# Kernel tuning notes

Hardware: AMD Instinct MI355X
Metric: run time of the kernel (lower is better)

## Reference

```python
import jax, jax.numpy as jnp
import numpy as np

B, S, E, H, SN, LMAX = 128, 512, 768, 16, 100, 5
DH = E // H  # 48

def setup_inputs() -> dict:
    key = jax.random.key(0)
    ks = jax.random.split(key, 10)
    idx = jax.random.randint(ks[0], (B, LMAX), 0, S)
    lengths = jax.random.randint(ks[1], (B,), 1, LMAX + 1)
    valid = jnp.arange(LMAX)[None, :] < lengths[:, None]
    locations = jnp.where(valid, idx, -1)
    return {
        "last_hidden_state": jax.random.normal(ks[2], (B, S, E), jnp.float32),
        "sense_emb": jax.random.normal(ks[3], (B, SN, E), jnp.float32),
        "locations": locations,
        "in_proj_weight": jax.random.normal(ks[4], (3 * E, E), jnp.float32) * 0.02,
        "in_proj_bias": jax.random.normal(ks[5], (3 * E,), jnp.float32) * 0.02,
        "out_proj_weight": jax.random.normal(ks[6], (E, E), jnp.float32) * 0.02,
        "out_proj_bias": jax.random.normal(ks[7], (E,), jnp.float32) * 0.02,
        "linear_weight": jax.random.normal(ks[8], (SN, E), jnp.float32) * 0.02,
        "linear_bias": jax.random.normal(ks[9], (SN,), jnp.float32) * 0.02,
    }

def reference(last_hidden_state, sense_emb, locations, in_proj_weight, in_proj_bias,
              out_proj_weight, out_proj_bias, linear_weight, linear_bias):
    # Ragged gather + mean over the valid (non -1) token locations per row.
    mask = (locations != -1)                                   # [B, LMAX]
    safe = jnp.where(mask, locations, 0)                       # [B, LMAX]
    gathered = jnp.take_along_axis(last_hidden_state, safe[..., None], axis=1)  # [B,LMAX,E]
    cnt = mask.sum(axis=1, keepdims=True).astype(last_hidden_state.dtype)
    pun = (gathered * mask[..., None]).sum(axis=1) / cnt       # [B, E]

    # qkv: prepend pun-word embedding to the sense embeddings -> [B, SN+1, E]
    qkv = jnp.concatenate([pun[:, None, :], sense_emb], axis=1)

    # nn.MultiheadAttention with batch_first=False: axis0 = seq (L=B), axis1 = batch (N=SN+1).
    proj = qkv @ in_proj_weight.T + in_proj_bias               # [L, N, 3E]
    q, k, v = jnp.split(proj, 3, axis=-1)
    L, N = qkv.shape[0], qkv.shape[1]
    q = q.reshape(L, N, H, DH) * (DH ** -0.5)
    k = k.reshape(L, N, H, DH)
    v = v.reshape(L, N, H, DH)
    scores = jnp.einsum('lnhd,mnhd->nhlm', q, k)               # [N,H,L,L]
    attn = jax.nn.softmax(scores, axis=-1)
    ctx = jnp.einsum('nhlm,mnhd->lnhd', attn, v).reshape(L, N, E)
    attn_out = ctx @ out_proj_weight.T + out_proj_bias         # [L, N, E]

    res = attn_out[:, 0, :]                                    # [B, E] (batch slot 0)
    res = res @ linear_weight.T + linear_bias                  # [B, SN]
    return res
```

## Files before the change

### kernel.cpp

```cpp
#include <hip/hip_runtime.h>

#define SEQ 512
#define EMB 768
#define K3E 2304
#define DHD 48

__global__ __launch_bounds__(256) void k0_pun(
    const float* __restrict__ lhs, const int* __restrict__ loc,
    float* __restrict__ pun)
{
  int id = blockIdx.x * 256 + threadIdx.x;
  int row = id / 192;
  int ch  = id - row * 192;
  int cnt = 0;
  float4 s = make_float4(0.f, 0.f, 0.f, 0.f);
#pragma unroll
  for (int j = 0; j < 5; j++) {
    int v = loc[row * 5 + j];
    if (v >= 0) {
      float4 wv = *(const float4*)&lhs[((size_t)row * SEQ + v) * EMB + ch * 4];
      s.x += wv.x; s.y += wv.y; s.z += wv.z; s.w += wv.w;
      cnt++;
    }
  }
  float inv = 1.0f / (float)cnt;
  *(float4*)&pun[(size_t)row * EMB + ch * 4] =
      make_float4(s.x * inv, s.y * inv, s.z * inv, s.w * inv);
}

__global__ __launch_bounds__(512, 4) void k1_gemm_wcomb(
    const float* __restrict__ pun, const float* __restrict__ Bw,
    const float* __restrict__ bias, float* __restrict__ C,
    const float* __restrict__ wlin, const float* __restrict__ wout,
    float* __restrict__ wcomb)
{
  __shared__ float lds[14336];
  const int t = threadIdx.x;
  const int w = t >> 6, l = t & 63;
  const int tx = l & 7, ty = l >> 3;
  const int gm = l & 15, gq = l >> 4;
  const int kbase = w * 96;
  const int AW = w * 1792, BW = AW + 640;

  float4 aF, bF0, bF1;
  float acc[2][4] = {};

#define STAGE_A(b) {                                                         \
    int Ab = AW + (b) * 320;                                                 \
    lds[Ab + (gq*4+0)*20 + gm] = aF.x;                                       \
    lds[Ab + (gq*4+1)*20 + gm] = aF.y;                                       \
    lds[Ab + (gq*4+2)*20 + gm] = aF.z;                                       \
    lds[Ab + (gq*4+3)*20 + gm] = aF.w; }

#define INNER(b) {                                                           \
    int Ab = AW + (b) * 320, Bb = BW + (b) * 576;                            \
    _Pragma("unroll")                                                        \
    for (int kk = 0; kk < 16; kk++) {                                        \
      float2 a  = *(float2*)&lds[Ab + kk * 20 + ty * 2];                     \
      float4 bb = *(float4*)&lds[Bb + kk * 36 + tx * 4];                     \
      acc[0][0] += a.x*bb.x; acc[0][1] += a.x*bb.y;                          \
      acc[0][2] += a.x*bb.z; acc[0][3] += a.x*bb.w;                          \
      acc[1][0] += a.y*bb.x; acc[1][1] += a.y*bb.y;                          \
      acc[1][2] += a.y*bb.z; acc[1][3] += a.y*bb.w;                          \
    } }

  if (blockIdx.x < 576) {
    const int c  = blockIdx.x;
    const int bm = (c / 72) * 16, bn = (c % 72) * 32;
    const int bl = l & 31, bh = l >> 5;
    const float* arow = pun + (size_t)(bm + gm) * EMB;
    const float* brow = Bw + (size_t)(bn + bl) * EMB;

#define G_LOAD(s) {                                                          \
    int k0 = kbase + (s) * 16;                                               \
    aF  = *(const float4*)&arow[k0 + gq * 4];                                \
    bF0 = *(const float4*)&brow[k0 + bh * 8 + 0];                            \
    bF1 = *(const float4*)&brow[k0 + bh * 8 + 4]; }

#define G_WRITE(b) {                                                         \
    STAGE_A(b)                                                               \
    int Bb = BW + (b) * 576;                                                 \
    lds[Bb + (bh*8+0)*36 + bl] = bF0.x; lds[Bb + (bh*8+1)*36 + bl] = bF0.y;  \
    lds[Bb + (bh*8+2)*36 + bl] = bF0.z; lds[Bb + (bh*8+3)*36 + bl] = bF0.w;  \
    lds[Bb + (bh*8+4)*36 + bl] = bF1.x; lds[Bb + (bh*8+5)*36 + bl] = bF1.y;  \
    lds[Bb + (bh*8+6)*36 + bl] = bF1.z; lds[Bb + (bh*8+7)*36 + bl] = bF1.w; }

    G_LOAD(0); G_WRITE(0);
    for (int s = 0; s < 6; s++) {
      int b = s & 1;
      if (s < 5) G_LOAD(s + 1);
      INNER(b);
      if (s < 5) G_WRITE(b ^ 1);
    }
#undef G_LOAD
#undef G_WRITE

#pragma unroll
    for (int i = 0; i < 2; i++)
      *(float4*)&lds[AW + (ty*2 + i) * 32 + tx * 4] =
          make_float4(acc[i][0], acc[i][1], acc[i][2], acc[i][3]);
    __syncthreads();
    int m = t >> 5, n = t & 31;
    float v = lds[0*1792 + t] + lds[1*1792 + t] + lds[2*1792 + t] + lds[3*1792 + t]
            + lds[4*1792 + t] + lds[5*1792 + t] + lds[6*1792 + t] + lds[7*1792 + t]
            + bias[bn + n];
    C[(size_t)(bm + m) * K3E + bn + n] = v;
  } else {
    const int cc = blockIdx.x - 576;
    const int bm = (cc / 24) * 16, bn = (cc % 24) * 32;
    const int wi = l >> 2;
    const int j4 = (l & 3) * 8;
    int arow_i = bm + gm; if (arow_i > 99) arow_i = 99;
    const float* arow = wlin + (size_t)arow_i * EMB;

#define W_LOAD(s) {                                                          \
    int k0 = kbase + (s) * 16;                                               \
    aF  = *(const float4*)&arow[k0 + gq * 4];                                \
    const float* wr = wout + (size_t)(k0 + wi) * EMB + bn + j4;              \
    bF0 = *(const float4*)&wr[0];                                            \
    bF1 = *(const float4*)&wr[4]; }

#define W_WRITE(b) {                                                         \
    STAGE_A(b)                                                               \
    int Bb = BW + (b) * 576;                                                 \
    *(float4*)&lds[Bb + wi*36 + j4]     = bF0;                               \
    *(float4*)&lds[Bb + wi*36 + j4 + 4] = bF1; }

    W_LOAD(0); W_WRITE(0);
    for (int s = 0; s < 6; s++) {
      int b = s & 1;
      if (s < 5) W_LOAD(s + 1);
      INNER(b);
      if (s < 5) W_WRITE(b ^ 1);
    }
#undef W_LOAD
#undef W_WRITE

#pragma unroll
    for (int i = 0; i < 2; i++)
      *(float4*)&lds[AW + (ty*2 + i) * 32 + tx * 4] =
          make_float4(acc[i][0], acc[i][1], acc[i][2], acc[i][3]);
    __syncthreads();
    int m = t >> 5, n = t & 31;
    if (bm + m < 100) {
      float v = lds[0*1792 + t] + lds[1*1792 + t] + lds[2*1792 + t] + lds[3*1792 + t]
              + lds[4*1792 + t] + lds[5*1792 + t] + lds[6*1792 + t] + lds[7*1792 + t];
      wcomb[(size_t)(bm + m) * EMB + bn + n] = v;
    }
  }
#undef STAGE_A
#undef INNER
}

__global__ __launch_bounds__(256) void k2_attn(
    const float* __restrict__ proj, float* __restrict__ ctx)
{
  __shared__ float ks[128][52];
  __shared__ float vs[128][52];
  int h  = blockIdx.x >> 3;
  int l0 = (blockIdx.x & 7) * 16;
  int t  = threadIdx.x;

  for (int i = t; i < 128 * 12; i += 256) {
    int m  = i / 12;
    int dd = (i - m * 12) * 4;
    float4 kv = *(const float4*)&proj[(size_t)m * K3E + EMB     + h * DHD + dd];
    float4 vv = *(const float4*)&proj[(size_t)m * K3E + 2 * EMB + h * DHD + dd];
    *(float4*)&ks[m][dd] = kv;
    *(float4*)&vs[m][dd] = vv;
  }

  int l  = t >> 4;
  int g  = t & 15;
  int lg = l0 + l;
  const float scale = 0.14433756729740643f;
  float q[48];
#pragma unroll
  for (int jj = 0; jj < 12; jj++) {
    float4 qv = *(const float4*)&proj[(size_t)lg * K3E + h * DHD + jj * 4];
    q[jj*4+0] = qv.x * scale; q[jj*4+1] = qv.y * scale;
    q[jj*4+2] = qv.z * scale; q[jj*4+3] = qv.w * scale;
  }
  __syncthreads();

  float sv[8];
  float smax = -1e30f;
#pragma unroll
  for (int jm = 0; jm < 8; jm++) {
    int m = g + jm * 16;
    float s = 0.0f;
#pragma unroll
    for (int dq = 0; dq < 12; dq++) {
      float4 kv = *(const float4*)&ks[m][dq * 4];
      s += q[dq*4+0]*kv.x + q[dq*4+1]*kv.y + q[dq*4+2]*kv.z + q[dq*4+3]*kv.w;
    }
    sv[jm] = s;
    smax = fmaxf(smax, s);
  }
#pragma unroll
  for (int off = 1; off < 16; off <<= 1) smax = fmaxf(smax, __shfl_xor(smax, off));
  float ssum = 0.0f;
#pragma unroll
  for (int jm = 0; jm < 8; jm++) { float e = __expf(sv[jm] - smax); sv[jm] = e; ssum += e; }
#pragma unroll
  for (int off = 1; off < 16; off <<= 1) ssum += __shfl_xor(ssum, off);
  float inv = 1.0f / ssum;
#pragma unroll
  for (int jm = 0; jm < 8; jm++) sv[jm] *= inv;

  float acc[48] = {};
#pragma unroll
  for (int jm = 0; jm < 8; jm++) {
    int m = g + jm * 16;
    float p = sv[jm];
#pragma unroll
    for (int dq = 0; dq < 12; dq++) {
      float4 vv = *(const float4*)&vs[m][dq * 4];
      acc[dq*4+0] += p*vv.x; acc[dq*4+1] += p*vv.y;
      acc[dq*4+2] += p*vv.z; acc[dq*4+3] += p*vv.w;
    }
  }

  {
    float buf[24];
    if (g & 8) {
#pragma unroll
      for (int d = 0; d < 24; d++) buf[d] = acc[d];
    } else {
#pragma unroll
      for (int d = 0; d < 24; d++) buf[d] = acc[d + 24];
    }
#pragma unroll
    for (int d = 0; d < 24; d++) buf[d] = __shfl_xor(buf[d], 8);
    if (g & 8) {
#pragma unroll
      for (int d = 0; d < 24; d++) acc[d] = acc[d + 24] + buf[d];
    } else {
#pragma unroll
      for (int d = 0; d < 24; d++) acc[d] = acc[d] + buf[d];
    }
  }
  {
    float buf[12];
    if (g & 4) {
#pragma unroll
      for (int d = 0; d < 12; d++) buf[d] = acc[d];
    } else {
#pragma unroll
      for (int d = 0; d < 12; d++) buf[d] = acc[d + 12];
    }
#pragma unroll
    for (int d = 0; d < 12; d++) buf[d] = __shfl_xor(buf[d], 4);
    if (g & 4) {
#pragma unroll
      for (int d = 0; d < 12; d++) acc[d] = acc[d + 12] + buf[d];
    } else {
#pragma unroll
      for (int d = 0; d < 12; d++) acc[d] = acc[d] + buf[d];
    }
  }
  {
    float buf[6];
    if (g & 2) {
#pragma unroll
      for (int d = 0; d < 6; d++) buf[d] = acc[d];
    } else {
#pragma unroll
      for (int d = 0; d < 6; d++) buf[d] = acc[d + 6];
    }
#pragma unroll
    for (int d = 0; d < 6; d++) buf[d] = __shfl_xor(buf[d], 2);
    if (g & 2) {
#pragma unroll
      for (int d = 0; d < 6; d++) acc[d] = acc[d + 6] + buf[d];
    } else {
#pragma unroll
      for (int d = 0; d < 6; d++) acc[d] = acc[d] + buf[d];
    }
  }
  {
    float buf[3];
    if (g & 1) {
#pragma unroll
      for (int d = 0; d < 3; d++) buf[d] = acc[d];
    } else {
#pragma unroll
      for (int d = 0; d < 3; d++) buf[d] = acc[d + 3];
    }
#pragma unroll
    for (int d = 0; d < 3; d++) buf[d] = __shfl_xor(buf[d], 1);
    if (g & 1) {
#pragma unroll
      for (int d = 0; d < 3; d++) acc[d] = acc[d + 3] + buf[d];
    } else {
#pragma unroll
      for (int d = 0; d < 3; d++) acc[d] = acc[d] + buf[d];
    }
  }
#pragma unroll
  for (int j = 0; j < 3; j++) {
    ctx[(size_t)lg * EMB + h * DHD + g * 3 + j] = acc[j];
  }
}

__global__ __launch_bounds__(512, 4) void k3_final(
    const float* __restrict__ A, const float* __restrict__ Bw,
    const float* __restrict__ wlin, const float* __restrict__ bout,
    const float* __restrict__ blin, float* __restrict__ C)
{
  __shared__ float lds[14368];
  const int t = threadIdx.x;
  const int w = t >> 6, l = t & 63;
  const int bm = blockIdx.y * 16, bn = blockIdx.x * 32;
  const int tx = l & 7, ty = l >> 3;
  const int gm = l & 15, gq = l >> 4;
  const int bl = l & 31, bh = l >> 5;
  const int kbase = w * 96;
  const int AW = w * 1792, BW = AW + 640;

  if (t < 256) {
    int col = bn + (t >> 3);
    int ks  = (t & 7) * 96;
    float p = 0.f;
    if (col < 100) {
      const float* wr = wlin + (size_t)col * EMB + ks;
#pragma unroll
      for (int j = 0; j < 24; j++) {
        float4 wv = *(const float4*)&wr[j * 4];
        float4 bv = *(const float4*)&bout[ks + j * 4];
        p += wv.x*bv.x + wv.y*bv.y + wv.z*bv.z + wv.w*bv.w;
      }
    }
    p += __shfl_xor(p, 1); p += __shfl_xor(p, 2); p += __shfl_xor(p, 4);
    if ((t & 7) == 0) lds[14336 + (t >> 3)] = p + (col < 100 ? blin[col] : 0.f);
  }

  const float* arow = A + (size_t)(bm + gm) * EMB;
  int brow_i = bn + bl; if (brow_i > 99) brow_i = 99;
  const float* brow = Bw + (size_t)brow_i * EMB;

  float4 aF, bF0, bF1;

#define F_LOAD(s) {                                                          \
    int k0 = kbase + (s) * 16;                                               \
    aF  = *(const float4*)&arow[k0 + gq * 4];                                \
    bF0 = *(const float4*)&brow[k0 + bh * 8 + 0];                            \
    bF1 = *(const float4*)&brow[k0 + bh * 8 + 4]; }

#define F_WRITE(b) {                                                         \
    int Ab = AW + (b) * 320;                                                 \
    lds[Ab + (gq*4+0)*20 + gm] = aF.x;                                       \
    lds[Ab + (gq*4+1)*20 + gm] = aF.y;                                       \
    lds[Ab + (gq*4+2)*20 + gm] = aF.z;                                       \
    lds[Ab + (gq*4+3)*20 + gm] = aF.w;                                       \
    int Bb = BW + (b) * 576;                                                 \
    lds[Bb + (bh*8+0)*36 + bl] = bF0.x; lds[Bb + (bh*8+1)*36 + bl] = bF0.y;  \
    lds[Bb + (bh*8+2)*36 + bl] = bF0.z; lds[Bb + (bh*8+3)*36 + bl] = bF0.w;  \
    lds[Bb + (bh*8+4)*36 + bl] = bF1.x; lds[Bb + (bh*8+5)*36 + bl] = bF1.y;  \
    lds[Bb + (bh*8+6)*36 + bl] = bF1.z; lds[Bb + (bh*8+7)*36 + bl] = bF1.w; }

  float acc[2][4] = {};
  F_LOAD(0); F_WRITE(0);
  for (int s = 0; s < 6; s++) {
    int b = s & 1;
    if (s < 5) F_LOAD(s + 1);
    int Ab = AW + b * 320, Bb = BW + b * 576;
#pragma unroll
    for (int kk = 0; kk < 16; kk++) {
      float2 a  = *(float2*)&lds[Ab + kk * 20 + ty * 2];
      float4 bb = *(float4*)&lds[Bb + kk * 36 + tx * 4];
      acc[0][0] += a.x*bb.x; acc[0][1] += a.x*bb.y; acc[0][2] += a.x*bb.z; acc[0][3] += a.x*bb.w;
      acc[1][0] += a.y*bb.x; acc[1][1] += a.y*bb.y; acc[1][2] += a.y*bb.z; acc[1][3] += a.y*bb.w;
    }
    if (s < 5) F_WRITE(b ^ 1);
  }
#undef F_LOAD
#undef F_WRITE

#pragma unroll
  for (int i = 0; i < 2; i++)
    *(float4*)&lds[AW + (ty*2 + i) * 32 + tx * 4] =
        make_float4(acc[i][0], acc[i][1], acc[i][2], acc[i][3]);
  __syncthreads();
  int m = t >> 5, n = t & 31;
  int col = bn + n;
  if (col < 100) {
    float v = lds[0*1792 + t] + lds[1*1792 + t] + lds[2*1792 + t] + lds[3*1792 + t]
            + lds[4*1792 + t] + lds[5*1792 + t] + lds[6*1792 + t] + lds[7*1792 + t]
            + lds[14336 + n];
    C[(size_t)(bm + m) * 100 + col] = v;
  }
}

extern "C" void kernel_launch(void* const* d_in, const int* in_sizes, int n_in,
                              void* d_out, int out_size, void* d_ws, size_t ws_size,
                              hipStream_t stream) {
  const float* lhs   = (const float*)d_in[0];
  const int*   loc   = (const int*)  d_in[2];
  const float* w_in  = (const float*)d_in[3];
  const float* b_in  = (const float*)d_in[4];
  const float* w_out = (const float*)d_in[5];
  const float* b_out = (const float*)d_in[6];
  const float* w_lin = (const float*)d_in[7];
  const float* b_lin = (const float*)d_in[8];
  float* out = (float*)d_out;

  char* ws = (char*)d_ws;
  float* pun   = (float*)(ws);
  float* proj  = (float*)(ws + 393216);
  float* ctx   = (float*)(ws + 393216 + 1179648);
  float* wcomb = (float*)(ws + 393216 + 1179648 + 393216);

  k0_pun<<<96, 256, 0, stream>>>(lhs, loc, pun);
  k1_gemm_wcomb<<<744, 512, 0, stream>>>(pun, w_in, b_in, proj,
                                         w_lin, w_out, wcomb);
  k2_attn<<<128, 256, 0, stream>>>(proj, ctx);
  k3_final<<<dim3(4, 8), 512, 0, stream>>>(ctx, wcomb, w_lin, b_out, b_lin, out);
}
```

Measured before the change: 45.93 us.

## Fuse attention and final GEMM into one launch with flag-based inter-block sync

Merges the attention kernel and the final projection GEMM into a single launch. Attention blocks, now 512 threads covering 32 query rows each, publish completion through atomic counters, and GEMM blocks spin on the counter for their row group before reading ctx. The combined output bias is moved into an extra block of the preceding GEMM kernel, and the flags are reset in the pun kernel. This removes one kernel launch and its idle gap, but the spin-wait relies on the attention blocks being scheduled alongside or before the waiting blocks.

```diff
diff --git a/kernel.cpp b/kernel.cpp
--- a/kernel.cpp
+++ b/kernel.cpp
@@ -7,8 +7,11 @@
 
 __global__ __launch_bounds__(256) void k0_pun(
     const float* __restrict__ lhs, const int* __restrict__ loc,
-    float* __restrict__ pun)
+    float* __restrict__ pun, int* __restrict__ flags)
 {
+  if (blockIdx.x == 0 && threadIdx.x < 4)
+    __hip_atomic_store(&flags[threadIdx.x], 0, __ATOMIC_RELAXED,
+                       __HIP_MEMORY_SCOPE_AGENT);
   int id = blockIdx.x * 256 + threadIdx.x;
   int row = id / 192;
   int ch  = id - row * 192;
@@ -32,13 +35,15 @@
     const float* __restrict__ pun, const float* __restrict__ Bw,
     const float* __restrict__ bias, float* __restrict__ C,
     const float* __restrict__ wlin, const float* __restrict__ wout,
-    float* __restrict__ wcomb)
+    const float* __restrict__ bout, const float* __restrict__ blin,
+    float* __restrict__ wcomb, float* __restrict__ wsbias)
 {
   __shared__ float lds[14336];
   const int t = threadIdx.x;
   const int w = t >> 6, l = t & 63;
   const int tx = l & 7, ty = l >> 3;
   const int gm = l & 15, gq = l >> 4;
+  const int bl = l & 31, bh = l >> 5;
   const int kbase = w * 96;
   const int AW = w * 1792, BW = AW + 640;
 
@@ -67,7 +72,6 @@
   if (blockIdx.x < 576) {
     const int c  = blockIdx.x;
     const int bm = (c / 72) * 16, bn = (c % 72) * 32;
-    const int bl = l & 31, bh = l >> 5;
     const float* arow = pun + (size_t)(bm + gm) * EMB;
     const float* brow = Bw + (size_t)(bn + bl) * EMB;
 
@@ -94,7 +98,6 @@
     }
 #undef G_LOAD
 #undef G_WRITE
-
 #pragma unroll
     for (int i = 0; i < 2; i++)
       *(float4*)&lds[AW + (ty*2 + i) * 32 + tx * 4] =
@@ -105,7 +108,7 @@
             + lds[4*1792 + t] + lds[5*1792 + t] + lds[6*1792 + t] + lds[7*1792 + t]
             + bias[bn + n];
     C[(size_t)(bm + m) * K3E + bn + n] = v;
-  } else {
+  } else if (blockIdx.x < 744) {
     const int cc = blockIdx.x - 576;
     const int bm = (cc / 24) * 16, bn = (cc % 24) * 32;
     const int wi = l >> 2;
@@ -135,7 +138,6 @@
     }
 #undef W_LOAD
 #undef W_WRITE
-
 #pragma unroll
     for (int i = 0; i < 2; i++)
       *(float4*)&lds[AW + (ty*2 + i) * 32 + tx * 4] =
@@ -147,199 +149,211 @@
               + lds[4*1792 + t] + lds[5*1792 + t] + lds[6*1792 + t] + lds[7*1792 + t];
       wcomb[(size_t)(bm + m) * EMB + bn + n] = v;
     }
+  } else {
+    if (t < 400) {
+      int col = t >> 2, q = t & 3;
+      const float* wr = wlin + (size_t)col * EMB + q * 192;
+      const float* br = bout + q * 192;
+      float p = 0.f;
+#pragma unroll
+      for (int j = 0; j < 48; j++) {
+        float4 wv = *(const float4*)&wr[j * 4];
+        float4 bv = *(const float4*)&br[j * 4];
+        p += wv.x*bv.x + wv.y*bv.y + wv.z*bv.z + wv.w*bv.w;
+      }
+      p += __shfl_xor(p, 1); p += __shfl_xor(p, 2);
+      if (q == 0) wsbias[col] = p + blin[col];
+    }
   }
 #undef STAGE_A
 #undef INNER
 }
 
-__global__ __launch_bounds__(256) void k2_attn(
-    const float* __restrict__ proj, float* __restrict__ ctx)
+__global__ __launch_bounds__(512, 4) void k23_attn_final(
+    const float* __restrict__ proj, const float* __restrict__ wcomb,
+    const float* __restrict__ wsbias, float* __restrict__ ctx,
+    float* __restrict__ out, int* __restrict__ flags)
 {
-  __shared__ float ks[128][52];
-  __shared__ float vs[128][52];
-  int h  = blockIdx.x >> 3;
-  int l0 = (blockIdx.x & 7) * 16;
-  int t  = threadIdx.x;
-
-  for (int i = t; i < 128 * 12; i += 256) {
-    int m  = i / 12;
-    int dd = (i - m * 12) * 4;
-    float4 kv = *(const float4*)&proj[(size_t)m * K3E + EMB     + h * DHD + dd];
-    float4 vv = *(const float4*)&proj[(size_t)m * K3E + 2 * EMB + h * DHD + dd];
-    *(float4*)&ks[m][dd] = kv;
-    *(float4*)&vs[m][dd] = vv;
-  }
-
-  int l  = t >> 4;
-  int g  = t & 15;
-  int lg = l0 + l;
-  const float scale = 0.14433756729740643f;
-  float q[48];
-#pragma unroll
-  for (int jj = 0; jj < 12; jj++) {
-    float4 qv = *(const float4*)&proj[(size_t)lg * K3E + h * DHD + jj * 4];
-    q[jj*4+0] = qv.x * scale; q[jj*4+1] = qv.y * scale;
-    q[jj*4+2] = qv.z * scale; q[jj*4+3] = qv.w * scale;
-  }
-  __syncthreads();
-
-  float sv[8];
-  float smax = -1e30f;
-#pragma unroll
-  for (int jm = 0; jm < 8; jm++) {
-    int m = g + jm * 16;
-    float s = 0.0f;
-#pragma unroll
-    for (int dq = 0; dq < 12; dq++) {
-      float4 kv = *(const float4*)&ks[m][dq * 4];
-      s += q[dq*4+0]*kv.x + q[dq*4+1]*kv.y + q[dq*4+2]*kv.z + q[dq*4+3]*kv.w;
-    }
-    sv[jm] = s;
-    smax = fmaxf(smax, s);
-  }
-#pragma unroll
-  for (int off = 1; off < 16; off <<= 1) smax = fmaxf(smax, __shfl_xor(smax, off));
-  float ssum = 0.0f;
-#pragma unroll
-  for (int jm = 0; jm < 8; jm++) { float e = __expf(sv[jm] - smax); sv[jm] = e; ssum += e; }
-#pragma unroll
-  for (int off = 1; off < 16; off <<= 1) ssum += __shfl_xor(ssum, off);
-  float inv = 1.0f / ssum;
-#pragma unroll
-  for (int jm = 0; jm < 8; jm++) sv[jm] *= inv;
-
-  float acc[48] = {};
-#pragma unroll
-  for (int jm = 0; jm < 8; jm++) {
-    int m = g + jm * 16;
-    float p = sv[jm];
-#pragma unroll
-    for (int dq = 0; dq < 12; dq++) {
-      float4 vv = *(const float4*)&vs[m][dq * 4];
-      acc[dq*4+0] += p*vv.x; acc[dq*4+1] += p*vv.y;
-      acc[dq*4+2] += p*vv.z; acc[dq*4+3] += p*vv.w;
-    }
-  }
-
-  {
-    float buf[24];
-    if (g & 8) {
-#pragma unroll
-      for (int d = 0; d < 24; d++) buf[d] = acc[d];
-    } else {
-#pragma unroll
-      for (int d = 0; d < 24; d++) buf[d] = acc[d + 24];
-    }
-#pragma unroll
-    for (int d = 0; d < 24; d++) buf[d] = __shfl_xor(buf[d], 8);
-    if (g & 8) {
-#pragma unroll
-      for (int d = 0; d < 24; d++) acc[d] = acc[d + 24] + buf[d];
-    } else {
-#pragma unroll
-      for (int d = 0; d < 24; d++) acc[d] = acc[d] + buf[d];
-    }
-  }
-  {
-    float buf[12];
-    if (g & 4) {
-#pragma unroll
-      for (int d = 0; d < 12; d++) buf[d] = acc[d];
-    } else {
-#pragma unroll
-      for (int d = 0; d < 12; d++) buf[d] = acc[d + 12];
-    }
-#pragma unroll
-    for (int d = 0; d < 12; d++) buf[d] = __shfl_xor(buf[d], 4);
-    if (g & 4) {
-#pragma unroll
-      for (int d = 0; d < 12; d++) acc[d] = acc[d + 12] + buf[d];
-    } else {
-#pragma unroll
-      for (int d = 0; d < 12; d++) acc[d] = acc[d] + buf[d];
-    }
-  }
-  {
-    float buf[6];
-    if (g & 2) {
-#pragma unroll
-      for (int d = 0; d < 6; d++) buf[d] = acc[d];
-    } else {
-#pragma unroll
-      for (int d = 0; d < 6; d++) buf[d] = acc[d + 6];
-    }
-#pragma unroll
-    for (int d = 0; d < 6; d++) buf[d] = __shfl_xor(buf[d], 2);
-    if (g & 2) {
-#pragma unroll
-      for (int d = 0; d < 6; d++) acc[d] = acc[d + 6] + buf[d];
-    } else {
-#pragma unroll
-      for (int d = 0; d < 6; d++) acc[d] = acc[d] + buf[d];
-    }
-  }
-  {
-    float buf[3];
-    if (g & 1) {
-#pragma unroll
-      for (int d = 0; d < 3; d++) buf[d] = acc[d];
-    } else {
-#pragma unroll
-      for (int d = 0; d < 3; d++) buf[d] = acc[d + 3];
-    }
-#pragma unroll
-    for (int d = 0; d < 3; d++) buf[d] = __shfl_xor(buf[d], 1);
-    if (g & 1) {
-#pragma unroll
-      for (int d = 0; d < 3; d++) acc[d] = acc[d + 3] + buf[d];
-    } else {
-#pragma unroll
-      for (int d = 0; d < 3; d++) acc[d] = acc[d] + buf[d];
-    }
-  }
-#pragma unroll
-  for (int j = 0; j < 3; j++) {
-    ctx[(size_t)lg * EMB + h * DHD + g * 3 + j] = acc[j];
-  }
-}
-
-__global__ __launch_bounds__(512, 4) void k3_final(
-    const float* __restrict__ A, const float* __restrict__ Bw,
-    const float* __restrict__ wlin, const float* __restrict__ bout,
-    const float* __restrict__ blin, float* __restrict__ C)
-{
-  __shared__ float lds[14368];
+  __shared__ float lds[14336];
   const int t = threadIdx.x;
-  const int w = t >> 6, l = t & 63;
-  const int bm = blockIdx.y * 16, bn = blockIdx.x * 32;
-  const int tx = l & 7, ty = l >> 3;
-  const int gm = l & 15, gq = l >> 4;
-  const int bl = l & 31, bh = l >> 5;
-  const int kbase = w * 96;
-  const int AW = w * 1792, BW = AW + 640;
-
-  if (t < 256) {
-    int col = bn + (t >> 3);
-    int ks  = (t & 7) * 96;
-    float p = 0.f;
-    if (col < 100) {
-      const float* wr = wlin + (size_t)col * EMB + ks;
-#pragma unroll
-      for (int j = 0; j < 24; j++) {
-        float4 wv = *(const float4*)&wr[j * 4];
-        float4 bv = *(const float4*)&bout[ks + j * 4];
-        p += wv.x*bv.x + wv.y*bv.y + wv.z*bv.z + wv.w*bv.w;
-      }
-    }
-    p += __shfl_xor(p, 1); p += __shfl_xor(p, 2); p += __shfl_xor(p, 4);
-    if ((t & 7) == 0) lds[14336 + (t >> 3)] = p + (col < 100 ? blin[col] : 0.f);
-  }
-
-  const float* arow = A + (size_t)(bm + gm) * EMB;
-  int brow_i = bn + bl; if (brow_i > 99) brow_i = 99;
-  const float* brow = Bw + (size_t)brow_i * EMB;
-
-  float4 aF, bF0, bF1;
+
+  if (blockIdx.x < 64) {
+    const int h  = blockIdx.x >> 2;
+    const int l0 = (blockIdx.x & 3) * 32;
+    float* ks = lds;
+    float* vs = lds + 6656;
+
+    for (int i = t; i < 128 * 12; i += 512) {
+      int m  = i / 12;
+      int dd = (i - m * 12) * 4;
+      float4 kv = *(const float4*)&proj[(size_t)m * K3E + EMB     + h * DHD + dd];
+      float4 vv = *(const float4*)&proj[(size_t)m * K3E + 2 * EMB + h * DHD + dd];
+      *(float4*)&ks[m * 52 + dd] = kv;
+      *(float4*)&vs[m * 52 + dd] = vv;
+    }
+
+    int lr = t >> 4;
+    int g  = t & 15;
+    int lg = l0 + lr;
+    const float scale = 0.14433756729740643f;
+    float q[48];
+#pragma unroll
+    for (int jj = 0; jj < 12; jj++) {
+      float4 qv = *(const float4*)&proj[(size_t)lg * K3E + h * DHD + jj * 4];
+      q[jj*4+0] = qv.x * scale; q[jj*4+1] = qv.y * scale;
+      q[jj*4+2] = qv.z * scale; q[jj*4+3] = qv.w * scale;
+    }
+    __syncthreads();
+
+    float sv[8];
+    float smax = -1e30f;
+#pragma unroll
+    for (int jm = 0; jm < 8; jm++) {
+      int m = g + jm * 16;
+      float s = 0.0f;
+#pragma unroll
+      for (int dq = 0; dq < 12; dq++) {
+        float4 kv = *(const float4*)&ks[m * 52 + dq * 4];
+        s += q[dq*4+0]*kv.x + q[dq*4+1]*kv.y + q[dq*4+2]*kv.z + q[dq*4+3]*kv.w;
+      }
+      sv[jm] = s;
+      smax = fmaxf(smax, s);
+    }
+#pragma unroll
+    for (int off = 1; off < 16; off <<= 1) smax = fmaxf(smax, __shfl_xor(smax, off));
+    float ssum = 0.0f;
+#pragma unroll
+    for (int jm = 0; jm < 8; jm++) { float e = __expf(sv[jm] - smax); sv[jm] = e; ssum += e; }
+#pragma unroll
+    for (int off = 1; off < 16; off <<= 1) ssum += __shfl_xor(ssum, off);
+    float inv = 1.0f / ssum;
+#pragma unroll
+    for (int jm = 0; jm < 8; jm++) sv[jm] *= inv;
+
+    float acc[48] = {};
+#pragma unroll
+    for (int jm = 0; jm < 8; jm++) {
+      int m = g + jm * 16;
+      float p = sv[jm];
+#pragma unroll
+      for (int dq = 0; dq < 12; dq++) {
+        float4 vv = *(const float4*)&vs[m * 52 + dq * 4];
+        acc[dq*4+0] += p*vv.x; acc[dq*4+1] += p*vv.y;
+        acc[dq*4+2] += p*vv.z; acc[dq*4+3] += p*vv.w;
+      }
+    }
+
+    {
+      float buf[24];
+      if (g & 8) {
+#pragma unroll
+        for (int d = 0; d < 24; d++) buf[d] = acc[d];
+      } else {
+#pragma unroll
+        for (int d = 0; d < 24; d++) buf[d] = acc[d + 24];
+      }
+#pragma unroll
+      for (int d = 0; d < 24; d++) buf[d] = __shfl_xor(buf[d], 8);
+      if (g & 8) {
+#pragma unroll
+        for (int d = 0; d < 24; d++) acc[d] = acc[d + 24] + buf[d];
+      } else {
+#pragma unroll
+        for (int d = 0; d < 24; d++) acc[d] = acc[d] + buf[d];
+      }
+    }
+    {
+      float buf[12];
+      if (g & 4) {
+#pragma unroll
+        for (int d = 0; d < 12; d++) buf[d] = acc[d];
+      } else {
+#pragma unroll
+        for (int d = 0; d < 12; d++) buf[d] = acc[d + 12];
+      }
+#pragma unroll
+      for (int d = 0; d < 12; d++) buf[d] = __shfl_xor(buf[d], 4);
+      if (g & 4) {
+#pragma unroll
+        for (int d = 0; d < 12; d++) acc[d] = acc[d + 12] + buf[d];
+      } else {
+#pragma unroll
+        for (int d = 0; d < 12; d++) acc[d] = acc[d] + buf[d];
+      }
+    }
+    {
+      float buf[6];
+      if (g & 2) {
+#pragma unroll
+        for (int d = 0; d < 6; d++) buf[d] = acc[d];
+      } else {
+#pragma unroll
+        for (int d = 0; d < 6; d++) buf[d] = acc[d + 6];
+      }
+#pragma unroll
+      for (int d = 0; d < 6; d++) buf[d] = __shfl_xor(buf[d], 2);
+      if (g & 2) {
+#pragma unroll
+        for (int d = 0; d < 6; d++) acc[d] = acc[d + 6] + buf[d];
+      } else {
+#pragma unroll
+        for (int d = 0; d < 6; d++) acc[d] = acc[d] + buf[d];
+      }
+    }
+    {
+      float buf[3];
+      if (g & 1) {
+#pragma unroll
+        for (int d = 0; d < 3; d++) buf[d] = acc[d];
+      } else {
+#pragma unroll
+        for (int d = 0; d < 3; d++) buf[d] = acc[d + 3];
+      }
+#pragma unroll
+      for (int d = 0; d < 3; d++) buf[d] = __shfl_xor(buf[d], 1);
+      if (g & 1) {
+#pragma unroll
+        for (int d = 0; d < 3; d++) acc[d] = acc[d + 3] + buf[d];
+      } else {
+#pragma unroll
+        for (int d = 0; d < 3; d++) acc[d] = acc[d] + buf[d];
+      }
+    }
+#pragma unroll
+    for (int j = 0; j < 3; j++) {
+      ctx[(size_t)lg * EMB + h * DHD + g * 3 + j] = acc[j];
+    }
+
+    __syncthreads();
+    if (t == 0) {
+      __threadfence();
+      __hip_atomic_fetch_add(&flags[l0 >> 5], 1, __ATOMIC_RELAXED,
+                             __HIP_MEMORY_SCOPE_AGENT);
+    }
+  } else {
+    const int c  = blockIdx.x - 64;
+    const int bm = (c >> 2) * 16, bn = (c & 3) * 32;
+
+    if (t == 0) {
+      while (__hip_atomic_load(&flags[bm >> 5], __ATOMIC_RELAXED,
+                               __HIP_MEMORY_SCOPE_AGENT) < 16)
+        __builtin_amdgcn_s_sleep(2);
+      __threadfence();
+    }
+    __syncthreads();
+
+    const int w = t >> 6, l = t & 63;
+    const int tx = l & 7, ty = l >> 3;
+    const int gm = l & 15, gq = l >> 4;
+    const int bl = l & 31, bh = l >> 5;
+    const int kbase = w * 96;
+    const int AW = w * 1792, BW = AW + 640;
+
+    const float* arow = ctx + (size_t)(bm + gm) * EMB;
+    int brow_i = bn + bl; if (brow_i > 99) brow_i = 99;
+    const float* brow = wcomb + (size_t)brow_i * EMB;
+
+    float4 aF, bF0, bF1;
 
 #define F_LOAD(s) {                                                          \
     int k0 = kbase + (s) * 16;                                               \
@@ -359,36 +373,37 @@
     lds[Bb + (bh*8+4)*36 + bl] = bF1.x; lds[Bb + (bh*8+5)*36 + bl] = bF1.y;  \
     lds[Bb + (bh*8+6)*36 + bl] = bF1.z; lds[Bb + (bh*8+7)*36 + bl] = bF1.w; }
 
-  float acc[2][4] = {};
-  F_LOAD(0); F_WRITE(0);
-  for (int s = 0; s < 6; s++) {
-    int b = s & 1;
-    if (s < 5) F_LOAD(s + 1);
-    int Ab = AW + b * 320, Bb = BW + b * 576;
-#pragma unroll
-    for (int kk = 0; kk < 16; kk++) {
-      float2 a  = *(float2*)&lds[Ab + kk * 20 + ty * 2];
-      float4 bb = *(float4*)&lds[Bb + kk * 36 + tx * 4];
-      acc[0][0] += a.x*bb.x; acc[0][1] += a.x*bb.y; acc[0][2] += a.x*bb.z; acc[0][3] += a.x*bb.w;
-      acc[1][0] += a.y*bb.x; acc[1][1] += a.y*bb.y; acc[1][2] += a.y*bb.z; acc[1][3] += a.y*bb.w;
-    }
-    if (s < 5) F_WRITE(b ^ 1);
-  }
+    float acc[2][4] = {};
+    F_LOAD(0); F_WRITE(0);
+    for (int s = 0; s < 6; s++) {
+      int b = s & 1;
+      if (s < 5) F_LOAD(s + 1);
+      int Ab = AW + b * 320, Bb = BW + b * 576;
+#pragma unroll
+      for (int kk = 0; kk < 16; kk++) {
+        float2 a  = *(float2*)&lds[Ab + kk * 20 + ty * 2];
+        float4 bb = *(float4*)&lds[Bb + kk * 36 + tx * 4];
+        acc[0][0] += a.x*bb.x; acc[0][1] += a.x*bb.y; acc[0][2] += a.x*bb.z; acc[0][3] += a.x*bb.w;
+        acc[1][0] += a.y*bb.x; acc[1][1] += a.y*bb.y; acc[1][2] += a.y*bb.z; acc[1][3] += a.y*bb.w;
+      }
+      if (s < 5) F_WRITE(b ^ 1);
+    }
 #undef F_LOAD
 #undef F_WRITE
 
 #pragma unroll
-  for (int i = 0; i < 2; i++)
-    *(float4*)&lds[AW + (ty*2 + i) * 32 + tx * 4] =
-        make_float4(acc[i][0], acc[i][1], acc[i][2], acc[i][3]);
-  __syncthreads();
-  int m = t >> 5, n = t & 31;
-  int col = bn + n;
-  if (col < 100) {
-    float v = lds[0*1792 + t] + lds[1*1792 + t] + lds[2*1792 + t] + lds[3*1792 + t]
-            + lds[4*1792 + t] + lds[5*1792 + t] + lds[6*1792 + t] + lds[7*1792 + t]
-            + lds[14336 + n];
-    C[(size_t)(bm + m) * 100 + col] = v;
+    for (int i = 0; i < 2; i++)
+      *(float4*)&lds[AW + (ty*2 + i) * 32 + tx * 4] =
+          make_float4(acc[i][0], acc[i][1], acc[i][2], acc[i][3]);
+    __syncthreads();
+    int m = t >> 5, n = t & 31;
+    int col = bn + n;
+    if (col < 100) {
+      float v = lds[0*1792 + t] + lds[1*1792 + t] + lds[2*1792 + t] + lds[3*1792 + t]
+              + lds[4*1792 + t] + lds[5*1792 + t] + lds[6*1792 + t] + lds[7*1792 + t]
+              + wsbias[col];
+      out[(size_t)(bm + m) * 100 + col] = v;
+    }
   }
 }
 
@@ -406,14 +421,16 @@
   float* out = (float*)d_out;
 
   char* ws = (char*)d_ws;
-  float* pun   = (float*)(ws);
-  float* proj  = (float*)(ws + 393216);
-  float* ctx   = (float*)(ws + 393216 + 1179648);
-  float* wcomb = (float*)(ws + 393216 + 1179648 + 393216);
-
-  k0_pun<<<96, 256, 0, stream>>>(lhs, loc, pun);
-  k1_gemm_wcomb<<<744, 512, 0, stream>>>(pun, w_in, b_in, proj,
-                                         w_lin, w_out, wcomb);
-  k2_attn<<<128, 256, 0, stream>>>(proj, ctx);
-  k3_final<<<dim3(4, 8), 512, 0, stream>>>(ctx, wcomb, w_lin, b_out, b_lin, out);
+  float* pun    = (float*)(ws);
+  float* proj   = (float*)(ws + 393216);
+  float* ctx    = (float*)(ws + 1572864);
+  float* wcomb  = (float*)(ws + 1966080);
+  float* wsbias = (float*)(ws + 2273280);
+  int*   flags  = (int*)  (ws + 2273680);
+
+  k0_pun<<<96, 256, 0, stream>>>(lhs, loc, pun, flags);
+  k1_gemm_wcomb<<<745, 512, 0, stream>>>(pun, w_in, b_in, proj,
+                                         w_lin, w_out, b_out, b_lin,
+                                         wcomb, wsbias);
+  k23_attn_final<<<96, 512, 0, stream>>>(proj, wcomb, wsbias, ctx, out, flags);
 }
```

New measurement: 59.56 us. +29.7%, slower.
